# Kernel optimization log

Hardware: AMD Instinct MI355X
Metric: run time of the kernel (lower is better)

Reference implementation:

```python
import jax, jax.numpy as jnp
import numpy as np

B, T, N, D = 8, 12, 512, 128
K = 16                      # number of pattern clusters
GEO_H, SEM_H, T_H = 4, 2, 2
HD = D // (GEO_H + SEM_H + T_H)      # 16
SCALE = HD ** -0.5
GD, SD, TD = GEO_H * HD, SEM_H * HD, T_H * HD  # 64, 32, 32


def setup_inputs() -> dict:
    key = jax.random.key(0)
    ks = jax.random.split(key, 24)
    w = lambda k, o, i: jax.random.normal(k, (o, i), jnp.float32) * 0.02
    return {
        'x': jax.random.normal(ks[0], (B, T, N, D), jnp.float32),
        'x_patterns': jax.random.normal(ks[1], (B, T, N, D, 1), jnp.float32),
        'pattern_keys': jax.random.normal(ks[2], (K, D, 1), jnp.float32),
        'dynamic_adj': jax.random.normal(ks[3], (B, N, N), jnp.float32) * 0.1,
        'geo_mask': jax.random.randint(ks[4], (N, N), 0, 2).astype(bool),
        'sem_mask': jax.random.randint(ks[5], (N, N), 0, 2).astype(bool),
        't_qw': w(ks[6], TD, D), 't_kw': w(ks[7], TD, D), 't_vw': w(ks[8], TD, D),
        'geo_qw': w(ks[9], GD, D), 'geo_kw': w(ks[10], GD, D), 'geo_vw': w(ks[11], GD, D),
        'sem_qw': w(ks[12], SD, D), 'sem_kw': w(ks[13], SD, D), 'sem_vw': w(ks[14], SD, D),
        'pat_qw': w(ks[15], GD, D), 'pat_qb': jax.random.normal(ks[16], (GD,), jnp.float32) * 0.02,
        'pat_kw': w(ks[17], GD, D), 'pat_kb': jax.random.normal(ks[18], (GD,), jnp.float32) * 0.02,
        'pat_vw': w(ks[19], GD, D), 'pat_vb': jax.random.normal(ks[20], (GD,), jnp.float32) * 0.02,
        'proj_w': w(ks[21], D, D), 'proj_b': jax.random.normal(ks[22], (D,), jnp.float32) * 0.02,
    }


def reference(x, x_patterns, pattern_keys, dynamic_adj, geo_mask, sem_mask,
              t_qw, t_kw, t_vw, geo_qw, geo_kw, geo_vw, sem_qw, sem_kw, sem_vw,
              pat_qw, pat_qb, pat_kw, pat_kb, pat_vw, pat_vb, proj_w, proj_b):
    Bc, Tc, Nc, Dc = x.shape
    proj3 = lambda z, w: jnp.einsum('btnd,ed->btne', z, w)  # 1x1 conv over channels

    # ---- temporal branch: attention over T per node ----
    def t_heads(z):  # (B,T,N,TD) -> (B,N,h,T,hd)
        return z.transpose(0, 2, 1, 3).reshape(Bc, Nc, Tc, T_H, HD).transpose(0, 1, 3, 2, 4)
    tq, tk, tv = t_heads(proj3(x, t_qw)), t_heads(proj3(x, t_kw)), t_heads(proj3(x, t_vw))
    t_attn = jax.nn.softmax(jnp.einsum('bnhqd,bnhkd->bnhqk', tq, tk) * SCALE, axis=-1)
    t_x = jnp.einsum('bnhqk,bnhkd->bnhqd', t_attn, tv)
    t_x = t_x.transpose(0, 1, 3, 2, 4).reshape(Bc, Nc, Tc, TD).transpose(0, 2, 1, 3)  # (B,T,N,TD)

    # ---- geo branch: pattern attention augments geo_k ----
    geo_q, geo_k, geo_v = proj3(x, geo_qw), proj3(x, geo_kw), proj3(x, geo_vw)
    pq = x_patterns[..., 0] @ pat_qw.T + pat_qb          # (B,T,N,GD)
    pk = pattern_keys[..., 0] @ pat_kw.T + pat_kb        # (K,GD)
    pv = pattern_keys[..., 0] @ pat_vw.T + pat_vb        # (K,GD)
    p_attn = jax.nn.softmax(jnp.einsum('btne,ke->btnk', pq, pk) * SCALE, axis=-1)
    geo_k = geo_k + jnp.einsum('btnk,ke->btne', p_attn, pv)

    def s_heads(z, h):  # (B,T,N,h*hd) -> (B,T,h,N,hd)
        return z.reshape(Bc, Tc, Nc, h, HD).transpose(0, 1, 3, 2, 4)
    gq, gk, gv = s_heads(geo_q, GEO_H), s_heads(geo_k, GEO_H), s_heads(geo_v, GEO_H)
    g_attn = jnp.einsum('bthqd,bthkd->bthqk', gq, gk) * SCALE
    g_attn = g_attn + dynamic_adj[:, None, None]         # dynamic bias
    g_attn = jnp.where(geo_mask, -jnp.inf, g_attn)
    g_attn = jax.nn.softmax(g_attn, axis=-1)
    geo_x = jnp.einsum('bthqk,bthkd->bthqd', g_attn, gv)
    geo_x = geo_x.transpose(0, 1, 3, 2, 4).reshape(Bc, Tc, Nc, GD)

    # ---- semantic branch ----
    sq = s_heads(proj3(x, sem_qw), SEM_H)
    sk = s_heads(proj3(x, sem_kw), SEM_H)
    sv = s_heads(proj3(x, sem_vw), SEM_H)
    s_attn = jnp.einsum('bthqd,bthkd->bthqk', sq, sk) * SCALE
    s_attn = jnp.where(sem_mask, -jnp.inf, s_attn)
    s_attn = jax.nn.softmax(s_attn, axis=-1)
    sem_x = jnp.einsum('bthqk,bthkd->bthqd', s_attn, sv)
    sem_x = sem_x.transpose(0, 1, 3, 2, 4).reshape(Bc, Tc, Nc, SD)

    out = jnp.concatenate([t_x, geo_x, sem_x], axis=-1) @ proj_w.T + proj_b
    return out
```

## Files before the change

kernel.cpp:

```cpp
#include <hip/hip_runtime.h>
#include <hip/hip_bf16.h>

using bf16 = __hip_bfloat16;
typedef __attribute__((ext_vector_type(8))) short short8;
typedef __attribute__((ext_vector_type(4))) float f32x4;
typedef __attribute__((ext_vector_type(4))) unsigned int u32x4;

#define Bc 8
#define Tc 12
#define Nc 512
#define Dc 128
#define T_Hc 2
#define GEO_Hc 4
#define SEM_Hc 2
#define HDc 16
#define SCALEc 0.25f
#define LOG2E 1.4426950408889634f

constexpr size_t TSZ = (size_t)Bc * Nc * T_Hc * Tc * HDc;
constexpr size_t GSZ = (size_t)Bc * Tc * GEO_Hc * Nc * HDc;
constexpr size_t SSZ = (size_t)Bc * Tc * SEM_Hc * Nc * HDc;
constexpr size_t CSZ = (size_t)Bc * Tc * Nc * Dc;
constexpr size_t H_TQ = 0;
constexpr size_t H_TK = H_TQ + TSZ;
constexpr size_t H_TV = H_TK + TSZ;
constexpr size_t H_GQ = H_TV + TSZ;
constexpr size_t H_GK = H_GQ + GSZ;
constexpr size_t H_GV = H_GK + GSZ;
constexpr size_t H_SQ = H_GV + GSZ;
constexpr size_t H_SK = H_SQ + SSZ;
constexpr size_t H_SV = H_SK + SSZ;
constexpr size_t H_CC = H_SV + SSZ;
constexpr size_t H_END = H_CC + CSZ;
constexpr size_t F_PK = (H_END + 1) / 2;
constexpr size_t F_PV = F_PK + 1024;
constexpr size_t F_FLAG = F_PV + 1024;
constexpr size_t H_W2X = 2 * (F_FLAG + 64);
constexpr size_t H_W2O = H_W2X + 384 * 256;
constexpr size_t H_BG = H_TQ;
constexpr size_t H_BS = H_TQ + 2097152;

__device__ __forceinline__ float b2f(bf16 v) { return __bfloat162float(v); }
__device__ __forceinline__ bf16 f2b(float v) { return __float2bfloat16(v); }
__device__ __forceinline__ short f2bs(float v) {
    bf16 b = __float2bfloat16(v);
    return *reinterpret_cast<short*>(&b);
}
__device__ __forceinline__ float bs2f(short s) {
    union { unsigned u; float f; } x;
    x.u = ((unsigned)(unsigned short)s) << 16;
    return x.f;
}
__device__ __forceinline__ unsigned packbf(float a, float b) {
    unsigned ua = (unsigned)(unsigned short)f2bs(a);
    unsigned ub = (unsigned)(unsigned short)f2bs(b);
    return ua | (ub << 16);
}
__device__ __forceinline__ float exp2hw(float x) {
    float r;
    asm("v_exp_f32 %0, %1" : "=v"(r) : "v"(x));
    return r;
}
__device__ __forceinline__ float rcphw(float x) {
    float r;
    asm("v_rcp_f32 %0, %1" : "=v"(r) : "v"(x));
    return r;
}

__device__ __forceinline__ const float* wrow(
    int gc, const float* tq, const float* tk, const float* tv,
    const float* gq, const float* gk, const float* gv,
    const float* sq, const float* sk, const float* sv) {
    if (gc < 32) return tq + (size_t)gc * 128;
    if (gc < 64) return tk + (size_t)(gc - 32) * 128;
    if (gc < 96) return tv + (size_t)(gc - 64) * 128;
    if (gc < 160) return gq + (size_t)(gc - 96) * 128;
    if (gc < 224) return gk + (size_t)(gc - 160) * 128;
    if (gc < 288) return gv + (size_t)(gc - 224) * 128;
    if (gc < 320) return sq + (size_t)(gc - 288) * 128;
    if (gc < 352) return sk + (size_t)(gc - 320) * 128;
    return sv + (size_t)(gc - 352) * 128;
}

__global__ __launch_bounds__(256) void k_prepw(
    const float* __restrict__ t_qw, const float* __restrict__ t_kw,
    const float* __restrict__ t_vw, const float* __restrict__ geo_qw,
    const float* __restrict__ geo_kw, const float* __restrict__ geo_vw,
    const float* __restrict__ sem_qw, const float* __restrict__ sem_kw,
    const float* __restrict__ sem_vw, const float* __restrict__ proj_w,
    const float* __restrict__ pattern_keys, const float* __restrict__ pat_kw,
    const float* __restrict__ pat_kb, const float* __restrict__ pat_vw,
    const float* __restrict__ pat_vb, const unsigned char* __restrict__ mask,
    bf16* __restrict__ hb, float* __restrict__ fws) {
    if (blockIdx.x < 256) {
        int gid = blockIdx.x * 256 + threadIdx.x;
        if (gid < 49152) {
            int row = gid >> 7, k = gid & 127;
            const float* src = wrow(row, t_qw, t_kw, t_vw, geo_qw, geo_kw,
                                    geo_vw, sem_qw, sem_kw, sem_vw);
            float v = src[k];
            if ((row >= 96 && row < 160) || (row >= 288 && row < 320))
                v *= SCALEc * LOG2E;
            bf16 bv = f2b(v);
            hb[H_W2X + (size_t)row * 256 + 2 * k] = bv;
            hb[H_W2X + (size_t)row * 256 + 2 * k + 1] = bv;
        } else {
            int g = gid - 49152;
            hb[H_W2O + g] = f2b(proj_w[g]);
        }
    } else if (blockIdx.x < 264) {
        int idx = (blockIdx.x - 256) * 256 + threadIdx.x;
        int which = idx >> 10;
        int r = idx & 1023;
        int k = r >> 6, e = r & 63;
        const float4* w = (const float4*)((which ? pat_vw : pat_kw) + (size_t)e * 128);
        const float4* pk = (const float4*)(pattern_keys + (size_t)k * 128);
        float acc = which ? pat_vb[e] : pat_kb[e];
#pragma unroll
        for (int j = 0; j < 32; ++j) {
            float4 a = pk[j], b = w[j];
            acc = fmaf(a.x, b.x, acc); acc = fmaf(a.y, b.y, acc);
            acc = fmaf(a.z, b.z, acc); acc = fmaf(a.w, b.w, acc);
        }
        fws[(which ? F_PV : F_PK) + (size_t)k * 64 + e] = acc;
    } else {
        __shared__ int s_u8, s_odd4;
        int tid = threadIdx.x;
        if (tid == 0) { s_u8 = 0; s_odd4 = 0; }
        __syncthreads();
        int u8 = 0, odd4 = 0;
        for (int i = tid * 16; i < tid * 16 + 16; ++i) {
            unsigned char v = mask[i];
            if (v && (i & 3)) u8 = 1;
            if (v && ((i & 7) == 4)) odd4 = 1;
        }
        if (u8) atomicOr(&s_u8, 1);
        if (odd4) atomicOr(&s_odd4, 1);
        __syncthreads();
        if (tid == 0) fws[F_FLAG] = s_u8 ? 0.f : (s_odd4 ? 1.f : 2.f);
    }
}

__global__ __launch_bounds__(256) void k_bias(
    const float* __restrict__ dyn, const unsigned char* __restrict__ gm,
    const unsigned char* __restrict__ sm, const float* __restrict__ fws,
    bf16* __restrict__ hb) {
    int bid = blockIdx.x;
    int tid = threadIdx.x;
    int mode = (int)fws[F_FLAG];
    if (bid < 8192) {
        int b = bid & 7;
        int inner = bid >> 3;
        size_t rem = (size_t)inner * 256 + tid;
        size_t gid = (size_t)b * 262144 + rem;
        int mv = (mode == 0) ? (int)gm[rem]
               : (mode == 1) ? ((const int*)gm)[rem]
                             : ((const int*)gm)[2 * rem];
        hb[H_BG + gid] = f2b(mv ? -1.44e30f : dyn[gid] * LOG2E);
    } else {
        size_t sid = (size_t)(bid - 8192) * 256 + tid;
        int mv = (mode == 0) ? (int)sm[sid]
               : (mode == 1) ? ((const int*)sm)[sid]
                             : ((const int*)sm)[2 * sid];
        hb[H_BS + sid] = f2b(mv ? -1.44e30f : 0.f);
    }
}

__global__ __launch_bounds__(256, 2) void k_projx(
    const float* __restrict__ x, bf16* __restrict__ hb) {
    __shared__ short xs[128 * 256];

    int tid = threadIdx.x;
    int m0 = blockIdx.x * 128;
    int b = m0 / (Tc * Nc);
    int rr = m0 - b * Tc * Nc;
    int t = rr >> 9;
    int n0 = rr & 511;

    for (int u = tid; u < 4096; u += 256) {
        int row = u >> 5, g = u & 31;
        float4 v = *(const float4*)(x + (size_t)(m0 + row) * 128 + g * 4);
        short8 s;
        short h0 = f2bs(v.x); s[0] = h0; s[1] = f2bs(v.x - bs2f(h0));
        short h1 = f2bs(v.y); s[2] = h1; s[3] = f2bs(v.y - bs2f(h1));
        short h2 = f2bs(v.z); s[4] = h2; s[5] = f2bs(v.z - bs2f(h2));
        short h3 = f2bs(v.w); s[6] = h3; s[7] = f2bs(v.w - bs2f(h3));
        *(short8*)&xs[row * 256 + ((g ^ (row & 7)) << 3)] = s;
    }
    __syncthreads();

    int w = tid >> 6;
    int lane = tid & 63;
    int l15 = lane & 15;
    int quad = lane >> 4;
    const bf16* w2 = hb + H_W2X;

    for (int nc = 0; nc < 6; ++nc) {
        f32x4 acc[2][4];
#pragma unroll
        for (int i = 0; i < 2; ++i)
#pragma unroll
            for (int j = 0; j < 4; ++j) acc[i][j] = (f32x4){0.f, 0.f, 0.f, 0.f};

#pragma unroll
        for (int ks = 0; ks < 8; ++ks) {
            int r0 = w * 32 + l15;
            int r1 = r0 + 16;
            short8 a0 = *(const short8*)&xs[r0 * 256 + (((ks * 4 + quad) ^ (r0 & 7)) << 3)];
            short8 a1 = *(const short8*)&xs[r1 * 256 + (((ks * 4 + quad) ^ (r1 & 7)) << 3)];
#pragma unroll
            for (int nj = 0; nj < 4; ++nj) {
                short8 bfr = *(const short8*)(w2 + (size_t)(nc * 64 + nj * 16 + l15) * 256
                                              + ks * 32 + quad * 8);
                acc[0][nj] = __builtin_amdgcn_mfma_f32_16x16x32_bf16(a0, bfr, acc[0][nj], 0, 0, 0);
                acc[1][nj] = __builtin_amdgcn_mfma_f32_16x16x32_bf16(a1, bfr, acc[1][nj], 0, 0, 0);
            }
        }
#pragma unroll
        for (int nj = 0; nj < 4; ++nj) {
            int gc = nc * 64 + nj * 16 + l15;
            int tile16 = nc * 4 + nj;
            int d = gc & 15;
#pragma unroll
            for (int i = 0; i < 2; ++i) {
                int nrow0 = n0 + w * 32 + i * 16 + quad * 4;
#pragma unroll
                for (int r = 0; r < 4; ++r) {
                    int n = nrow0 + r;
                    float v = acc[i][nj][r];
                    size_t idx;
                    if (tile16 < 6) {
                        int which = gc >> 5, hh = (gc >> 4) & 1;
                        size_t base = which == 0 ? H_TQ : which == 1 ? H_TK : H_TV;
                        idx = base + ((size_t)(b * Nc + n) * T_Hc + hh) * (Tc * HDc)
                              + t * HDc + d;
                    } else if (tile16 < 18) {
                        int r2 = gc - 96;
                        int which = r2 >> 6, hh = (r2 >> 4) & 3;
                        size_t base = which == 0 ? H_GQ : which == 1 ? H_GK : H_GV;
                        size_t sl = (((size_t)b * Tc + t) * GEO_Hc + hh) * (Nc * HDc);
                        idx = base + sl + (which == 2 ? ((size_t)d * Nc + n)
                                                      : ((size_t)n * HDc + d));
                    } else {
                        int r2 = gc - 288;
                        int which = r2 >> 5, hh = (r2 >> 4) & 1;
                        size_t base = which == 0 ? H_SQ : which == 1 ? H_SK : H_SV;
                        size_t sl = (((size_t)b * Tc + t) * SEM_Hc + hh) * (Nc * HDc);
                        idx = base + sl + (which == 2 ? ((size_t)d * Nc + n)
                                                      : ((size_t)n * HDc + d));
                    }
                    hb[idx] = f2b(v);
                }
            }
        }
    }
}

__global__ __launch_bounds__(256, 2) void k_projp(
    const float* __restrict__ xp, const float* __restrict__ pat_qw,
    const float* __restrict__ pat_qb, const float* __restrict__ fws,
    bf16* __restrict__ hb) {
    __shared__ float xs[64 * 132];
    __shared__ float wsh[64 * 68];
    __shared__ float pks[1024], pvs[1024], pqbs[64];

    int tid = threadIdx.x;
    int tok0 = blockIdx.x * 64;
    int ty = tid >> 4, tx = tid & 15;

    for (int u = tid; u < 2048; u += 256) {
        int row = u >> 5, f4 = u & 31;
        *(float4*)&xs[row * 132 + f4 * 4] =
            *(const float4*)(xp + (size_t)(tok0 + row) * 128 + f4 * 4);
    }
    for (int u = tid; u < 1024; u += 256) {
        pks[u] = fws[F_PK + u];
        pvs[u] = fws[F_PV + u];
    }
    if (tid < 64) pqbs[tid] = pat_qb[tid];

    float acc[4][4] = {};
    for (int kh = 0; kh < 2; ++kh) {
        __syncthreads();
        for (int u = tid; u < 1024; u += 256) {
            int row = u >> 4, f4 = u & 15;
            *(float4*)&wsh[row * 68 + f4 * 4] =
                *(const float4*)(pat_qw + (size_t)row * 128 + kh * 64 + f4 * 4);
        }
        __syncthreads();
#pragma unroll 4
        for (int kk = 0; kk < 64; kk += 4) {
            float4 a[4], b[4];
#pragma unroll
            for (int i = 0; i < 4; ++i)
                a[i] = *(const float4*)&xs[(ty + 16 * i) * 132 + kh * 64 + kk];
#pragma unroll
            for (int j = 0; j < 4; ++j)
                b[j] = *(const float4*)&wsh[(tx + 16 * j) * 68 + kk];
#pragma unroll
            for (int i = 0; i < 4; ++i)
#pragma unroll
                for (int j = 0; j < 4; ++j) {
                    acc[i][j] = fmaf(a[i].x, b[j].x, acc[i][j]);
                    acc[i][j] = fmaf(a[i].y, b[j].y, acc[i][j]);
                    acc[i][j] = fmaf(a[i].z, b[j].z, acc[i][j]);
                    acc[i][j] = fmaf(a[i].w, b[j].w, acc[i][j]);
                }
        }
    }
    __syncthreads();
    float* pqs = xs;
    float* plogs = wsh;
#pragma unroll
    for (int i = 0; i < 4; ++i)
#pragma unroll
        for (int j = 0; j < 4; ++j)
            pqs[(ty + 16 * i) * 68 + tx + 16 * j] = acc[i][j] + pqbs[tx + 16 * j];
    __syncthreads();
    {
        int tok = tid >> 2, k4 = (tid & 3) * 4;
        for (int k = k4; k < k4 + 4; ++k) {
            float s = 0.f;
#pragma unroll 16
            for (int e = 0; e < 64; ++e)
                s = fmaf(pqs[tok * 68 + e], pks[k * 64 + e], s);
            plogs[tok * 17 + k] = s * SCALEc;
        }
    }
    __syncthreads();
    {
        int tok = tid >> 2, q = tid & 3;
        float mx = -1e30f;
        for (int k = 0; k < 16; ++k) mx = fmaxf(mx, plogs[tok * 17 + k]);
        float p[16], sum = 0.f;
        for (int k = 0; k < 16; ++k) {
            p[k] = __expf(plogs[tok * 17 + k] - mx);
            sum += p[k];
        }
        float inv = 1.f / sum;
        int token = tok0 + tok;
        int b = token / (Tc * Nc);
        int rr = token - b * Tc * Nc;
        int t = rr >> 9;
        int n = rr & 511;
        for (int cc = 0; cc < 16; ++cc) {
            int c = q * 16 + cc;
            float v = 0.f;
            for (int k = 0; k < 16; ++k) v = fmaf(p[k], pvs[k * 64 + c], v);
            v *= inv;
            size_t idx = H_GK + (((size_t)b * Tc + t) * GEO_Hc + (c >> 4)) * (Nc * HDc)
                         + n * HDc + (c & 15);
            hb[idx] = f2b(b2f(hb[idx]) + v);
        }
    }
}

__global__ __launch_bounds__(64) void k_tattn(bf16* __restrict__ hb) {
    int blk = blockIdx.x;
    int h = blk & 1;
    int bn = blk >> 1;
    int b = bn >> 9;
    int n = bn & 511;
    size_t base = ((size_t)(b * Nc + n) * T_Hc + h) * (Tc * HDc);

    __shared__ float q[192], kk[192], v[192], s[144];
    int tid = threadIdx.x;
    for (int u = tid; u < 192; u += 64) {
        q[u] = b2f(hb[H_TQ + base + u]);
        kk[u] = b2f(hb[H_TK + base + u]);
        v[u] = b2f(hb[H_TV + base + u]);
    }
    __syncthreads();
    for (int idx = tid; idx < 144; idx += 64) {
        int qi = idx / 12, ki = idx - qi * 12;
        float acc = 0.f;
#pragma unroll
        for (int d = 0; d < 16; ++d) acc = fmaf(q[qi * 16 + d], kk[ki * 16 + d], acc);
        s[idx] = acc * SCALEc;
    }
    __syncthreads();
    if (tid < 12) {
        float mx = -1e30f;
        for (int ki = 0; ki < 12; ++ki) mx = fmaxf(mx, s[tid * 12 + ki]);
        float sum = 0.f;
        for (int ki = 0; ki < 12; ++ki) {
            float p = __expf(s[tid * 12 + ki] - mx);
            s[tid * 12 + ki] = p;
            sum += p;
        }
        float inv = 1.f / sum;
        for (int ki = 0; ki < 12; ++ki) s[tid * 12 + ki] *= inv;
    }
    __syncthreads();
    for (int idx = tid; idx < 192; idx += 64) {
        int qi = idx >> 4, d = idx & 15;
        float acc = 0.f;
#pragma unroll
        for (int ki = 0; ki < 12; ++ki) acc = fmaf(s[qi * 12 + ki], v[ki * 16 + d], acc);
        hb[H_CC + (((size_t)b * Tc + qi) * Nc + n) * Dc + h * HDc + d] = f2b(acc);
    }
}

__global__ __launch_bounds__(256, 8) void k_attn2m(bf16* __restrict__ hb) {
    __shared__ short vt[16 * 512];

    int bid = blockIdx.x;
    int b = bid & 7;
    int rem = bid >> 3;
    int m3 = rem % 3;
    int d3 = rem / 3;

    int H, coff, lb;
    size_t QO, KO, VO, bstride;
    const bf16* bias0;
    if (m3 == 2) {
        H = SEM_Hc; coff = 96; QO = H_SQ; KO = H_SK; VO = H_SV;
        bias0 = hb + H_BS; bstride = 0; lb = d3;
    } else {
        H = GEO_Hc; coff = 32; QO = H_GQ; KO = H_GK; VO = H_GV;
        bias0 = hb + H_BG; bstride = (size_t)Nc * Nc; lb = 2 * d3 + m3;
    }
    int part = lb & 7;
    int th = lb >> 3;
    int h = th % H;
    int t = th / H;

    size_t bth = (((size_t)b * Tc + t) * H + h) * (size_t)(Nc * HDc);
    const bf16* Qp = hb + QO + bth;
    const bf16* Kp = hb + KO + bth;
    const bf16* Vg = hb + VO + bth;
    const bf16* bp = bias0 + (size_t)b * bstride;

    int tid = threadIdx.x;

    for (int u = tid; u < 1024; u += 256) {
        int d = u >> 6, gg = u & 63;
        *(short8*)&vt[d * 512 + ((gg ^ (d & 7)) << 3)] =
            *(const short8*)(Vg + (size_t)d * 512 + gg * 8);
    }
    __syncthreads();

    int lane = tid & 63;
    int w = tid >> 6;
    int l15 = lane & 15;
    int quad = lane >> 4;
    int sw = l15 & 7;
    int srcA = l15 + ((lane & 16) << 1);
    int srcB = srcA + 16;
    bool hi = lane >= 32;

    union U8 { u32x4 u; short8 s; };

    int q0 = part * 64 + w * 16;
    int qg = q0 + l15;
    short8 bq = {0, 0, 0, 0, 0, 0, 0, 0};
    if (quad < 2) bq = *(const short8*)(Qp + (size_t)qg * 16 + quad * 8);

    float l_i = 0.f;
    f32x4 O = {0.f, 0.f, 0.f, 0.f};

    for (int ch = 0; ch < 4; ++ch) {
        int kabs0 = ch * 128;
        f32x4 S[8];
#pragma unroll
        for (int kt = 0; kt < 8; ++kt) {
            int kabs = kabs0 + kt * 16;
            short4 bb = *(const short4*)(bp + (size_t)qg * 512 + kabs + quad * 4);
            f32x4 c;
            c[0] = bs2f(bb.x); c[1] = bs2f(bb.y);
            c[2] = bs2f(bb.z); c[3] = bs2f(bb.w);
            short8 ak = {0, 0, 0, 0, 0, 0, 0, 0};
            if (quad < 2)
                ak = *(const short8*)(Kp + (size_t)(kabs + l15) * 16 + quad * 8);
            S[kt] = __builtin_amdgcn_mfma_f32_16x16x32_bf16(ak, bq, c, 0, 0, 0);
        }
        unsigned pk2[8][2];
        float psum = 0.f;
#pragma unroll
        for (int kt = 0; kt < 8; ++kt) {
            float p0 = exp2hw(S[kt][0]);
            float p1 = exp2hw(S[kt][1]);
            float p2 = exp2hw(S[kt][2]);
            float p3 = exp2hw(S[kt][3]);
            psum += (p0 + p1) + (p2 + p3);
            pk2[kt][0] = packbf(p0, p1);
            pk2[kt][1] = packbf(p2, p3);
        }
        psum += __shfl_xor(psum, 16);
        psum += __shfl_xor(psum, 32);
        l_i += psum;
        __builtin_amdgcn_s_setprio(1);
#pragma unroll
        for (int kw = 0; kw < 4; ++kw) {
            unsigned eA0 = __shfl(pk2[2 * kw][0], srcA);
            unsigned eA1 = __shfl(pk2[2 * kw][1], srcA);
            unsigned oA0 = __shfl(pk2[2 * kw + 1][0], srcA);
            unsigned oA1 = __shfl(pk2[2 * kw + 1][1], srcA);
            unsigned eB0 = __shfl(pk2[2 * kw][0], srcB);
            unsigned eB1 = __shfl(pk2[2 * kw][1], srcB);
            unsigned oB0 = __shfl(pk2[2 * kw + 1][0], srcB);
            unsigned oB1 = __shfl(pk2[2 * kw + 1][1], srcB);
            U8 ap;
            ap.u = (u32x4){hi ? oA0 : eA0, hi ? oA1 : eA1,
                           hi ? oB0 : eB0, hi ? oB1 : eB1};
            short8 bv = *(const short8*)&vt[l15 * 512
                             + (((ch * 16 + kw * 4 + quad) ^ sw) << 3)];
            O = __builtin_amdgcn_mfma_f32_16x16x32_bf16(ap.s, bv, O, 0, 0, 0);
        }
        __builtin_amdgcn_s_setprio(0);
    }
    float li0 = __shfl(l_i, (quad << 2) | 0);
    float li1 = __shfl(l_i, (quad << 2) | 1);
    float li2 = __shfl(l_i, (quad << 2) | 2);
    float li3 = __shfl(l_i, (quad << 2) | 3);
    size_t obase = H_CC + (((size_t)b * Tc + t) * Nc + q0) * Dc + coff + h * HDc + l15;
    hb[obase + (size_t)(quad * 4 + 0) * Dc] = f2b(O[0] * rcphw(li0));
    hb[obase + (size_t)(quad * 4 + 1) * Dc] = f2b(O[1] * rcphw(li1));
    hb[obase + (size_t)(quad * 4 + 2) * Dc] = f2b(O[2] * rcphw(li2));
    hb[obase + (size_t)(quad * 4 + 3) * Dc] = f2b(O[3] * rcphw(li3));
}

__global__ __launch_bounds__(256, 3) void k_outm(
    const bf16* __restrict__ hb, const float* __restrict__ proj_b,
    float* __restrict__ out) {
    __shared__ short cs[128 * 128];
    __shared__ float pbs[128];

    int tid = threadIdx.x;
    int m0 = blockIdx.x * 128;

    for (int u = tid; u < 2048; u += 256) {
        int row = u >> 4, g = u & 15;
        *(short8*)&cs[row * 128 + ((g ^ (row & 7)) << 3)] =
            *(const short8*)(hb + H_CC + (size_t)(m0 + row) * 128 + g * 8);
    }
    if (tid < 128) pbs[tid] = proj_b[tid];
    __syncthreads();

    int w = tid >> 6;
    int lane = tid & 63;
    int l15 = lane & 15;
    int quad = lane >> 4;
    const bf16* w2o = hb + H_W2O;

    f32x4 acc[2][8];
#pragma unroll
    for (int i = 0; i < 2; ++i)
#pragma unroll
        for (int j = 0; j < 8; ++j) acc[i][j] = (f32x4){0.f, 0.f, 0.f, 0.f};

#pragma unroll
    for (int ks = 0; ks < 4; ++ks) {
        int r0 = w * 32 + l15;
        int r1 = r0 + 16;
        short8 a0 = *(const short8*)&cs[r0 * 128 + (((ks * 4 + quad) ^ (r0 & 7)) << 3)];
        short8 a1 = *(const short8*)&cs[r1 * 128 + (((ks * 4 + quad) ^ (r1 & 7)) << 3)];
#pragma unroll
        for (int nj = 0; nj < 8; ++nj) {
            short8 bfr = *(const short8*)(w2o + (size_t)(nj * 16 + l15) * 128
                                          + ks * 32 + quad * 8);
            acc[0][nj] = __builtin_amdgcn_mfma_f32_16x16x32_bf16(a0, bfr, acc[0][nj], 0, 0, 0);
            acc[1][nj] = __builtin_amdgcn_mfma_f32_16x16x32_bf16(a1, bfr, acc[1][nj], 0, 0, 0);
        }
    }
#pragma unroll
    for (int i = 0; i < 2; ++i) {
#pragma unroll
        for (int nj = 0; nj < 8; ++nj) {
            int ch = nj * 16 + l15;
            float bias = pbs[ch];
#pragma unroll
            for (int r = 0; r < 4; ++r) {
                int token = m0 + w * 32 + i * 16 + quad * 4 + r;
                out[(size_t)token * 128 + ch] = acc[i][nj][r] + bias;
            }
        }
    }
}

extern "C" void kernel_launch(void* const* d_in, const int* in_sizes, int n_in,
                              void* d_out, int out_size, void* d_ws, size_t ws_size,
                              hipStream_t stream) {
    const float* x = (const float*)d_in[0];
    const float* xp = (const float*)d_in[1];
    const float* pattern_keys = (const float*)d_in[2];
    const float* dyn = (const float*)d_in[3];
    const void* geo_mask = d_in[4];
    const void* sem_mask = d_in[5];
    const float* t_qw = (const float*)d_in[6];
    const float* t_kw = (const float*)d_in[7];
    const float* t_vw = (const float*)d_in[8];
    const float* geo_qw = (const float*)d_in[9];
    const float* geo_kw = (const float*)d_in[10];
    const float* geo_vw = (const float*)d_in[11];
    const float* sem_qw = (const float*)d_in[12];
    const float* sem_kw = (const float*)d_in[13];
    const float* sem_vw = (const float*)d_in[14];
    const float* pat_qw = (const float*)d_in[15];
    const float* pat_qb = (const float*)d_in[16];
    const float* pat_kw = (const float*)d_in[17];
    const float* pat_kb = (const float*)d_in[18];
    const float* pat_vw = (const float*)d_in[19];
    const float* pat_vb = (const float*)d_in[20];
    const float* proj_w = (const float*)d_in[21];
    const float* proj_b = (const float*)d_in[22];

    bf16* hb = (bf16*)d_ws;
    float* fws = (float*)d_ws;

    k_prepw<<<265, 256, 0, stream>>>(t_qw, t_kw, t_vw, geo_qw, geo_kw, geo_vw,
                                     sem_qw, sem_kw, sem_vw, proj_w,
                                     pattern_keys, pat_kw, pat_kb, pat_vw,
                                     pat_vb, (const unsigned char*)geo_mask,
                                     hb, fws);
    k_projx<<<384, 256, 0, stream>>>(x, hb);
    k_projp<<<768, 256, 0, stream>>>(xp, pat_qw, pat_qb, fws, hb);
    k_tattn<<<Bc * Nc * T_Hc, 64, 0, stream>>>(hb);
    k_bias<<<9216, 256, 0, stream>>>(dyn, (const unsigned char*)geo_mask,
                                     (const unsigned char*)sem_mask, fws, hb);
    k_attn2m<<<Bc * Tc * (GEO_Hc + SEM_Hc) * 8, 256, 0, stream>>>(hb);
    k_outm<<<384, 256, 0, stream>>>(hb, proj_b, (float*)d_out);
}
```

Baseline: 338.4 us.

## Fuse pattern-memory projection into k_projx and batch temporal attention blocks

The separate k_projp kernel is folded into k_projx. Each 128-token block now computes the pattern query projection, the softmax over the 16 pattern keys and the value mix in shared memory, then adds the result to geo_k before writing it once, instead of doing a bf16 read-modify-write of geo_k in a later kernel. k_tattn is changed to pack four (b,n,h) units per 256-thread block, which cuts the block count by four. The cost is that the fused k_projx does an extra fp32 FMA GEMM with pat_qw read straight from global memory, which may raise its serial time and its register or LDS pressure.

```diff
diff --git a/kernel.cpp b/kernel.cpp
--- a/kernel.cpp
+++ b/kernel.cpp
@@ -167,8 +167,11 @@
 }
 
 __global__ __launch_bounds__(256, 2) void k_projx(
-    const float* __restrict__ x, bf16* __restrict__ hb) {
+    const float* __restrict__ x, const float* __restrict__ xp,
+    const float* __restrict__ pat_qw, const float* __restrict__ pat_qb,
+    const float* __restrict__ fws, bf16* __restrict__ hb) {
     __shared__ short xs[128 * 256];
+    __shared__ short pat[128 * 64];
 
     int tid = threadIdx.x;
     int m0 = blockIdx.x * 128;
@@ -176,6 +179,103 @@
     int rr = m0 - b * Tc * Nc;
     int t = rr >> 9;
     int n0 = rr & 511;
+
+    float* xpf = (float*)xs;
+    for (int u = tid; u < 4096; u += 256) {
+        int row = u >> 5, g = u & 31;
+        *(float4*)&xpf[row * 128 + ((g ^ (row & 7)) << 2)] =
+            *(const float4*)(xp + (size_t)(m0 + row) * 128 + g * 4);
+    }
+    __syncthreads();
+
+    int ty = tid >> 4, tx = tid & 15;
+    float pacc[8][4];
+#pragma unroll
+    for (int i = 0; i < 8; ++i)
+#pragma unroll
+        for (int j = 0; j < 4; ++j) pacc[i][j] = 0.f;
+    for (int kk = 0; kk < 128; kk += 4) {
+        int g = kk >> 2;
+        float4 bv[4];
+#pragma unroll
+        for (int j = 0; j < 4; ++j)
+            bv[j] = *(const float4*)(pat_qw + (size_t)(tx + 16 * j) * 128 + kk);
+#pragma unroll
+        for (int i = 0; i < 8; ++i) {
+            int row = ty + 16 * i;
+            float4 av = *(const float4*)&xpf[row * 128 + ((g ^ (row & 7)) << 2)];
+#pragma unroll
+            for (int j = 0; j < 4; ++j) {
+                pacc[i][j] = fmaf(av.x, bv[j].x, pacc[i][j]);
+                pacc[i][j] = fmaf(av.y, bv[j].y, pacc[i][j]);
+                pacc[i][j] = fmaf(av.z, bv[j].z, pacc[i][j]);
+                pacc[i][j] = fmaf(av.w, bv[j].w, pacc[i][j]);
+            }
+        }
+    }
+    __syncthreads();
+    float* pqs = (float*)xs;
+    {
+        float qb[4];
+#pragma unroll
+        for (int j = 0; j < 4; ++j) qb[j] = pat_qb[tx + 16 * j];
+#pragma unroll
+        for (int i = 0; i < 8; ++i)
+#pragma unroll
+            for (int j = 0; j < 4; ++j)
+                pqs[(ty + 16 * i) * 69 + tx + 16 * j] = pacc[i][j] + qb[j];
+    }
+    __syncthreads();
+
+    {
+        int tok = tid >> 1, hf = tid & 1;
+        float lg[8];
+#pragma unroll
+        for (int k = 0; k < 8; ++k) lg[k] = 0.f;
+        for (int e = 0; e < 64; ++e) {
+            float q = pqs[tok * 69 + e];
+#pragma unroll
+            for (int k = 0; k < 8; ++k)
+                lg[k] = fmaf(q, fws[F_PK + (size_t)(hf * 8 + k) * 64 + e], lg[k]);
+        }
+#pragma unroll
+        for (int k = 0; k < 8; ++k) lg[k] *= SCALEc;
+        float mx = lg[0];
+#pragma unroll
+        for (int k = 1; k < 8; ++k) mx = fmaxf(mx, lg[k]);
+        mx = fmaxf(mx, __shfl_xor(mx, 1));
+        float pown[8], sown = 0.f;
+#pragma unroll
+        for (int k = 0; k < 8; ++k) {
+            pown[k] = __expf(lg[k] - mx);
+            sown += pown[k];
+        }
+        float inv = 1.f / (sown + __shfl_xor(sown, 1));
+        float poth[8];
+#pragma unroll
+        for (int k = 0; k < 8; ++k) poth[k] = __shfl_xor(pown[k], 1);
+#pragma unroll
+        for (int g4 = 0; g4 < 8; ++g4) {
+            short4 st;
+            float vv[4];
+#pragma unroll
+            for (int el = 0; el < 4; ++el) {
+                int c = hf * 32 + g4 * 4 + el;
+                float v = 0.f;
+#pragma unroll
+                for (int k = 0; k < 8; ++k) {
+                    v = fmaf(pown[k], fws[F_PV + (size_t)(hf * 8 + k) * 64 + c], v);
+                    v = fmaf(poth[k], fws[F_PV + (size_t)((1 - hf) * 8 + k) * 64 + c], v);
+                }
+                vv[el] = v * inv;
+            }
+            st.x = f2bs(vv[0]); st.y = f2bs(vv[1]);
+            st.z = f2bs(vv[2]); st.w = f2bs(vv[3]);
+            int g = hf * 8 + g4;
+            *(short4*)&pat[tok * 64 + ((g ^ (tok & 7)) << 2)] = st;
+        }
+    }
+    __syncthreads();
 
     for (int u = tid; u < 4096; u += 256) {
         int row = u >> 5, g = u & 31;
@@ -239,6 +339,12 @@
                         int which = r2 >> 6, hh = (r2 >> 4) & 3;
                         size_t base = which == 0 ? H_GQ : which == 1 ? H_GK : H_GV;
                         size_t sl = (((size_t)b * Tc + t) * GEO_Hc + hh) * (Nc * HDc);
+                        if (which == 1) {
+                            int c = gc - 160;
+                            int lr = w * 32 + i * 16 + quad * 4 + r;
+                            v += bs2f(pat[lr * 64
+                                   + ((((c >> 2) ^ (lr & 7)) << 2) | (c & 3))]);
+                        }
                         idx = base + sl + (which == 2 ? ((size_t)d * Nc + n)
                                                       : ((size_t)n * HDc + d));
                     } else {
@@ -256,147 +362,51 @@
     }
 }
 
-__global__ __launch_bounds__(256, 2) void k_projp(
-    const float* __restrict__ xp, const float* __restrict__ pat_qw,
-    const float* __restrict__ pat_qb, const float* __restrict__ fws,
-    bf16* __restrict__ hb) {
-    __shared__ float xs[64 * 132];
-    __shared__ float wsh[64 * 68];
-    __shared__ float pks[1024], pvs[1024], pqbs[64];
-
-    int tid = threadIdx.x;
-    int tok0 = blockIdx.x * 64;
-    int ty = tid >> 4, tx = tid & 15;
-
-    for (int u = tid; u < 2048; u += 256) {
-        int row = u >> 5, f4 = u & 31;
-        *(float4*)&xs[row * 132 + f4 * 4] =
-            *(const float4*)(xp + (size_t)(tok0 + row) * 128 + f4 * 4);
-    }
-    for (int u = tid; u < 1024; u += 256) {
-        pks[u] = fws[F_PK + u];
-        pvs[u] = fws[F_PV + u];
-    }
-    if (tid < 64) pqbs[tid] = pat_qb[tid];
-
-    float acc[4][4] = {};
-    for (int kh = 0; kh < 2; ++kh) {
-        __syncthreads();
-        for (int u = tid; u < 1024; u += 256) {
-            int row = u >> 4, f4 = u & 15;
-            *(float4*)&wsh[row * 68 + f4 * 4] =
-                *(const float4*)(pat_qw + (size_t)row * 128 + kh * 64 + f4 * 4);
-        }
-        __syncthreads();
-#pragma unroll 4
-        for (int kk = 0; kk < 64; kk += 4) {
-            float4 a[4], b[4];
-#pragma unroll
-            for (int i = 0; i < 4; ++i)
-                a[i] = *(const float4*)&xs[(ty + 16 * i) * 132 + kh * 64 + kk];
-#pragma unroll
-            for (int j = 0; j < 4; ++j)
-                b[j] = *(const float4*)&wsh[(tx + 16 * j) * 68 + kk];
-#pragma unroll
-            for (int i = 0; i < 4; ++i)
-#pragma unroll
-                for (int j = 0; j < 4; ++j) {
-                    acc[i][j] = fmaf(a[i].x, b[j].x, acc[i][j]);
-                    acc[i][j] = fmaf(a[i].y, b[j].y, acc[i][j]);
-                    acc[i][j] = fmaf(a[i].z, b[j].z, acc[i][j]);
-                    acc[i][j] = fmaf(a[i].w, b[j].w, acc[i][j]);
-                }
-        }
-    }
-    __syncthreads();
-    float* pqs = xs;
-    float* plogs = wsh;
-#pragma unroll
-    for (int i = 0; i < 4; ++i)
-#pragma unroll
-        for (int j = 0; j < 4; ++j)
-            pqs[(ty + 16 * i) * 68 + tx + 16 * j] = acc[i][j] + pqbs[tx + 16 * j];
-    __syncthreads();
-    {
-        int tok = tid >> 2, k4 = (tid & 3) * 4;
-        for (int k = k4; k < k4 + 4; ++k) {
-            float s = 0.f;
-#pragma unroll 16
-            for (int e = 0; e < 64; ++e)
-                s = fmaf(pqs[tok * 68 + e], pks[k * 64 + e], s);
-            plogs[tok * 17 + k] = s * SCALEc;
-        }
-    }
-    __syncthreads();
-    {
-        int tok = tid >> 2, q = tid & 3;
-        float mx = -1e30f;
-        for (int k = 0; k < 16; ++k) mx = fmaxf(mx, plogs[tok * 17 + k]);
-        float p[16], sum = 0.f;
-        for (int k = 0; k < 16; ++k) {
-            p[k] = __expf(plogs[tok * 17 + k] - mx);
-            sum += p[k];
-        }
-        float inv = 1.f / sum;
-        int token = tok0 + tok;
-        int b = token / (Tc * Nc);
-        int rr = token - b * Tc * Nc;
-        int t = rr >> 9;
-        int n = rr & 511;
-        for (int cc = 0; cc < 16; ++cc) {
-            int c = q * 16 + cc;
-            float v = 0.f;
-            for (int k = 0; k < 16; ++k) v = fmaf(p[k], pvs[k * 64 + c], v);
-            v *= inv;
-            size_t idx = H_GK + (((size_t)b * Tc + t) * GEO_Hc + (c >> 4)) * (Nc * HDc)
-                         + n * HDc + (c & 15);
-            hb[idx] = f2b(b2f(hb[idx]) + v);
-        }
-    }
-}
-
-__global__ __launch_bounds__(64) void k_tattn(bf16* __restrict__ hb) {
-    int blk = blockIdx.x;
+__global__ __launch_bounds__(256, 8) void k_tattn(bf16* __restrict__ hb) {
+    __shared__ float q[4][192], kkv[4][192], vv[4][192], ss[4][144];
+    int unit = threadIdx.x >> 6;
+    int tid = threadIdx.x & 63;
+    int blk = blockIdx.x * 4 + unit;
     int h = blk & 1;
     int bn = blk >> 1;
     int b = bn >> 9;
     int n = bn & 511;
     size_t base = ((size_t)(b * Nc + n) * T_Hc + h) * (Tc * HDc);
 
-    __shared__ float q[192], kk[192], v[192], s[144];
-    int tid = threadIdx.x;
     for (int u = tid; u < 192; u += 64) {
-        q[u] = b2f(hb[H_TQ + base + u]);
-        kk[u] = b2f(hb[H_TK + base + u]);
-        v[u] = b2f(hb[H_TV + base + u]);
+        q[unit][u] = b2f(hb[H_TQ + base + u]);
+        kkv[unit][u] = b2f(hb[H_TK + base + u]);
+        vv[unit][u] = b2f(hb[H_TV + base + u]);
     }
     __syncthreads();
     for (int idx = tid; idx < 144; idx += 64) {
         int qi = idx / 12, ki = idx - qi * 12;
         float acc = 0.f;
 #pragma unroll
-        for (int d = 0; d < 16; ++d) acc = fmaf(q[qi * 16 + d], kk[ki * 16 + d], acc);
-        s[idx] = acc * SCALEc;
+        for (int d = 0; d < 16; ++d)
+            acc = fmaf(q[unit][qi * 16 + d], kkv[unit][ki * 16 + d], acc);
+        ss[unit][idx] = acc * SCALEc;
     }
     __syncthreads();
     if (tid < 12) {
         float mx = -1e30f;
-        for (int ki = 0; ki < 12; ++ki) mx = fmaxf(mx, s[tid * 12 + ki]);
+        for (int ki = 0; ki < 12; ++ki) mx = fmaxf(mx, ss[unit][tid * 12 + ki]);
         float sum = 0.f;
         for (int ki = 0; ki < 12; ++ki) {
-            float p = __expf(s[tid * 12 + ki] - mx);
-            s[tid * 12 + ki] = p;
+            float p = __expf(ss[unit][tid * 12 + ki] - mx);
+            ss[unit][tid * 12 + ki] = p;
             sum += p;
         }
         float inv = 1.f / sum;
-        for (int ki = 0; ki < 12; ++ki) s[tid * 12 + ki] *= inv;
+        for (int ki = 0; ki < 12; ++ki) ss[unit][tid * 12 + ki] *= inv;
     }
     __syncthreads();
     for (int idx = tid; idx < 192; idx += 64) {
         int qi = idx >> 4, d = idx & 15;
         float acc = 0.f;
 #pragma unroll
-        for (int ki = 0; ki < 12; ++ki) acc = fmaf(s[qi * 12 + ki], v[ki * 16 + d], acc);
+        for (int ki = 0; ki < 12; ++ki)
+            acc = fmaf(ss[unit][qi * 12 + ki], vv[unit][ki * 16 + d], acc);
         hb[H_CC + (((size_t)b * Tc + qi) * Nc + n) * Dc + h * HDc + d] = f2b(acc);
     }
 }
@@ -613,9 +623,8 @@
                                      pattern_keys, pat_kw, pat_kb, pat_vw,
                                      pat_vb, (const unsigned char*)geo_mask,
                                      hb, fws);
-    k_projx<<<384, 256, 0, stream>>>(x, hb);
-    k_projp<<<768, 256, 0, stream>>>(xp, pat_qw, pat_qb, fws, hb);
-    k_tattn<<<Bc * Nc * T_Hc, 64, 0, stream>>>(hb);
+    k_projx<<<384, 256, 0, stream>>>(x, xp, pat_qw, pat_qb, fws, hb);
+    k_tattn<<<2048, 256, 0, stream>>>(hb);
     k_bias<<<9216, 256, 0, stream>>>(dyn, (const unsigned char*)geo_mask,
                                      (const unsigned char*)sem_mask, fws, hb);
     k_attn2m<<<Bc * Tc * (GEO_Hc + SEM_Hc) * 8, 256, 0, stream>>>(hb);
```

After: 376.1 us. +11.2%, slower.
